# Kernel tuning notes

Measured on AMD Instinct MI355X. Metric: run time of the kernel, lower is better.

## Reference

```python
import jax, jax.numpy as jnp
import numpy as np

DIM = 128
B, H, W = 2, 256, 256


def conv2d(x, w, b, groups=1):
    # x: [B,C,H,W], w: [O, C//groups, kh, kw] (OIHW)
    y = jax.lax.conv_general_dilated(
        x, w, window_strides=(1, 1), padding='SAME',
        dimension_numbers=('NCHW', 'OIHW', 'NCHW'),
        feature_group_count=groups)
    return y + b[None, :, None, None]


def l2_normalize(x, axis=-1, eps=1e-12):
    # matches torch.nn.functional.normalize (p=2)
    n = jnp.sqrt(jnp.sum(x * x, axis=axis, keepdims=True))
    return x / jnp.maximum(n, eps)


def setup_inputs() -> dict:
    key = jax.random.key(0)
    ks = jax.random.split(key, 14)
    d = DIM
    h = d // 2
    s = 0.05
    return {
        'x': jax.random.normal(ks[0], (B, d, H, W), dtype=jnp.float32),
        'w_qkv': jax.random.normal(ks[1], (3 * d, d, 1, 1), dtype=jnp.float32) * s,
        'b_qkv': jax.random.normal(ks[2], (3 * d,), dtype=jnp.float32) * s,
        'w_q': jax.random.normal(ks[3], (d, 1, 3, 3), dtype=jnp.float32) * s,
        'b_q': jax.random.normal(ks[4], (d,), dtype=jnp.float32) * s,
        'w_k': jax.random.normal(ks[5], (d, 1, 3, 3), dtype=jnp.float32) * s,
        'b_k': jax.random.normal(ks[6], (d,), dtype=jnp.float32) * s,
        'w_v1': jax.random.normal(ks[7], (h, 2, 3, 3), dtype=jnp.float32) * s,  # groups=d/2, 2 in-ch per group
        'b_v1': jax.random.normal(ks[8], (h,), dtype=jnp.float32) * s,
        'w_v2': jax.random.normal(ks[9], (h, 1, 3, 3), dtype=jnp.float32) * s,  # depthwise on d/2
        'b_v2': jax.random.normal(ks[10], (h,), dtype=jnp.float32) * s,
        'temperature': jnp.ones((d, 1, 1), dtype=jnp.float32),
        'w_po': jax.random.normal(ks[11], (d, d, 1, 1), dtype=jnp.float32) * s,
        'b_po': jax.random.normal(ks[12], (d,), dtype=jnp.float32) * s,
    }


def reference(x, w_qkv, b_qkv, w_q, b_q, w_k, b_k, w_v1, b_v1, w_v2, b_v2,
              temperature, w_po, b_po):
    d = x.shape[1]
    h = d // 2
    # 1x1 conv -> qkv, then split
    qkv = conv2d(x, w_qkv, b_qkv)                     # [B,3d,H,W]
    q, k, v = jnp.split(qkv, 3, axis=1)
    # depthwise 3x3 on q, k
    q = conv2d(q, w_q, b_q, groups=d)
    k = conv2d(k, w_k, b_k, groups=d)
    # MDC on v: grouped conv (2->1 per group), depthwise, concat, sigmoid gate
    x1 = conv2d(v, w_v1, b_v1, groups=h)              # [B,d/2,H,W]
    x2 = conv2d(x1, w_v2, b_v2, groups=h)             # [B,d/2,H,W]
    v = jax.nn.sigmoid(v) * jnp.concatenate([x1, x2], axis=1)
    # per-channel row attention: normalize over W, [B,C,H,H] scores
    q1 = l2_normalize(q, axis=-1)
    k1 = l2_normalize(k, axis=-1)
    scores = jnp.einsum('bchw,bcgw->bchg', q1, k1) * temperature[None]  # [B,C,H,H]
    attn = jax.nn.softmax(scores, axis=-1)
    out = jnp.einsum('bchg,bcgw->bchw', attn, v)      # [B,C,H,W]
    return conv2d(out, w_po, b_po)
```

## Files before the change

### kernel.cpp

```cpp
#include <hip/hip_runtime.h>

typedef unsigned short u16;
typedef unsigned int u32;

#define HW 256
#define PIX 65536

#define WS_T1   100663296ull
#define WS_K1   134217728ull
#define WS_VP   167772160ull
#define WS_NEED 201326592ull

typedef __attribute__((ext_vector_type(8))) short s8v;
typedef __attribute__((ext_vector_type(4))) float f4v;

__device__ __forceinline__ float bu2f(u16 u){ union{u32 i; float f;} x; x.i=((u32)u)<<16; return x.f; }
__device__ __forceinline__ u16 f2bu(float f){ union{float f; u32 i;} x; x.f=f; u32 i=x.i; return (u16)((i + 0x7FFFu + ((i>>16)&1u))>>16); }
__device__ __forceinline__ float sigm(float x){ return 1.0f/(1.0f+__expf(-x)); }
__device__ __forceinline__ u16 cvt_el(float v){ return f2bu(v); }
__device__ __forceinline__ u16 cvt_el(u16 v){ return v; }
__device__ __forceinline__ int swz(int r, int c){ return r*256 + (((c>>3) ^ (r&7))<<3) + (c&7); }
__device__ __forceinline__ int pswz(int p, int c){ return (p<<7) + (((c>>3) ^ (p&7))<<3) + (c&7); }
__device__ __forceinline__ int vt_el(int w, int gb){
  int q = (w & 15) ^ gb ^ ((w >> 4) & 7);
  return ((w >> 4) << 10) + (gb << 7) + (q << 3);
}

__global__ __launch_bounds__(256) void k_wprep(const float* __restrict__ Wg, u16* __restrict__ G, int n){
  int i = blockIdx.x * 256 + threadIdx.x;
  if (i >= n) return;
  int o = i >> 7, c = i & 127;
  G[(o << 7) | (c ^ ((o & 7) << 3))] = f2bu(Wg[i]);
}

template<int OC, typename TIN, bool F32>
__global__ __launch_bounds__(512,1) void k_gemmP2(const TIN* __restrict__ in, const u16* __restrict__ Wbf,
                                                  const float* __restrict__ bias, int O_total,
                                                  void* __restrict__ outv){
  extern __shared__ u16 lds[];
  u16* Wl = lds;
  u16* Xl = lds + OC*128;
  int t = threadIdx.x;
  {
    const uint4* Wq4 = (const uint4*)Wbf;
    uint4* Wl4 = (uint4*)Wl;
    #pragma unroll
    for (int i = t; i < OC*16; i += 512) Wl4[i] = Wq4[i];
  }
  int p_blk = blockIdx.x * 256;
  int b = p_blk >> 16;
  int p0 = p_blk & 65535;
  if (sizeof(TIN) == 4){
    int p = t & 255, half = (t >> 8) * 64;
    const float* col = (const float*)in + ((size_t)(b*128 + half))*PIX + p0 + p;
    #pragma unroll
    for (int c8 = 0; c8 < 8; ++c8){
      u32 pk[4];
      #pragma unroll
      for (int j = 0; j < 4; ++j){
        u16 v0 = f2bu(col[(size_t)(c8*8 + 2*j)*PIX]);
        u16 v1 = f2bu(col[(size_t)(c8*8 + 2*j + 1)*PIX]);
        pk[j] = (u32)v0 | ((u32)v1 << 16);
      }
      *(uint4*)(Xl + pswz(p, half + c8*8)) = make_uint4(pk[0],pk[1],pk[2],pk[3]);
    }
  } else {
    int p = (t & 127) * 2, quarter = (t >> 7) * 32;
    const u16* col = (const u16*)in + ((size_t)(b*128 + quarter))*PIX + p0 + p;
    #pragma unroll
    for (int c8 = 0; c8 < 4; ++c8){
      u32 va[4], vb[4];
      #pragma unroll
      for (int j = 0; j < 4; ++j){
        u32 w0 = *(const u32*)(col + (size_t)(c8*8 + 2*j)*PIX);
        u32 w1 = *(const u32*)(col + (size_t)(c8*8 + 2*j + 1)*PIX);
        va[j] = (w0 & 0xFFFFu) | (w1 << 16);
        vb[j] = (w0 >> 16) | (w1 & 0xFFFF0000u);
      }
      *(uint4*)(Xl + pswz(p,     quarter + c8*8)) = make_uint4(va[0],va[1],va[2],va[3]);
      *(uint4*)(Xl + pswz(p + 1, quarter + c8*8)) = make_uint4(vb[0],vb[1],vb[2],vb[3]);
    }
  }
  __syncthreads();

  int wv = t >> 6, l = t & 63;
  int lg = l >> 4, lr = l & 15;
  int p_in0 = p0 + wv*32 + lr;

  s8v bf[2][4];
  #pragma unroll
  for (int pt = 0; pt < 2; ++pt){
    int p = wv*32 + pt*16 + lr;
    #pragma unroll
    for (int ks = 0; ks < 4; ++ks)
      bf[pt][ks] = *(const s8v*)(Xl + pswz(p, ks*32 + lg*8));
  }

  for (int ot = 0; ot < OC / 16; ++ot){
    f4v acc[2];
    acc[0] = (f4v){0.f,0.f,0.f,0.f};
    acc[1] = (f4v){0.f,0.f,0.f,0.f};
    int o = (ot << 4) + lr;
    const u16* wl = Wl + (o << 7);
    int sw = (o & 7) << 3;
    #pragma unroll
    for (int ks = 0; ks < 4; ++ks){
      s8v a = *(const s8v*)(wl + ((((ks << 5) + (lg << 3)) ^ sw)));
      acc[0] = __builtin_amdgcn_mfma_f32_16x16x32_bf16(a, bf[0][ks], acc[0], 0, 0, 0);
      acc[1] = __builtin_amdgcn_mfma_f32_16x16x32_bf16(a, bf[1][ks], acc[1], 0, 0, 0);
    }
    #pragma unroll
    for (int j = 0; j < 4; ++j){
      int o_row = (ot << 4) + (lg << 2) + j;
      float bv = bias[o_row];
      size_t base = ((size_t)(b * O_total + o_row)) << 16;
      #pragma unroll
      for (int pt = 0; pt < 2; ++pt){
        if (F32){
          ((float*)outv)[base + p_in0 + pt*16] = acc[pt][j] + bv;
        } else {
          ((u16*)outv)[base + p_in0 + pt*16] = f2bu(acc[pt][j] + bv);
        }
      }
    }
  }
}
#define GP384_LDS ((384*128 + 256*128) * 2)
#define GP128_LDS ((128*128 + 256*128) * 2)

__global__ __launch_bounds__(256) void k_dwqk2(const u16* __restrict__ qkv,
                                               const float* __restrict__ w_q, const float* __restrict__ b_q,
                                               const float* __restrict__ w_k, const float* __restrict__ b_k,
                                               u16* __restrict__ q1, u16* __restrict__ k1){
  __shared__ u16 ins[18*272];
  int t = threadIdx.x;
  int chunk = blockIdx.x;
  int c = blockIdx.y;
  int which = blockIdx.z & 1, b = blockIdx.z >> 1;
  const u16* in = qkv + ((size_t)(b*384 + which*128 + c)) * PIX;

  #pragma unroll
  for (int i = t; i < 612; i += 256) ((uint4*)ins)[i] = make_uint4(0,0,0,0);
  __syncthreads();
  int r0 = chunk*16 - 1;
  for (int i = t; i < 576; i += 256){
    int j = i >> 5, k = i & 31;
    int r = r0 + j;
    if (r >= 0 && r < HW)
      *(uint4*)(ins + j*272 + 8 + k*8) = *(const uint4*)(in + r*HW + k*8);
  }
  __syncthreads();

  const float* wk = (which ? w_k : w_q) + c*9;
  float K0=wk[0],K1=wk[1],K2=wk[2],K3=wk[3],K4=wk[4],K5=wk[5],K6=wk[6],K7=wk[7],K8=wk[8];
  float bias = (which ? b_k : b_q)[c];

  int wv = t >> 6, l = t & 63;
  int cb = l * 4;
  float wr[3][6];
  auto ldrow = [&](int j, int slot){
    ushort4 m = *(const ushort4*)(ins + j*272 + 8 + cb);
    wr[slot][0] = bu2f(ins[j*272 + 7 + cb]);
    wr[slot][1] = bu2f(m.x); wr[slot][2] = bu2f(m.y);
    wr[slot][3] = bu2f(m.z); wr[slot][4] = bu2f(m.w);
    wr[slot][5] = bu2f(ins[j*272 + 12 + cb]);
  };
  int rb = wv * 4;
  ldrow(rb, 0); ldrow(rb+1, 1);
  u16* outp = (which ? k1 : q1) + ((size_t)(b*128 + c)) * PIX;
  #pragma unroll
  for (int s = 0; s < 4; ++s){
    ldrow(rb + s + 2, (s+2)%3);
    const float* T = wr[s%3];
    const float* M = wr[(s+1)%3];
    const float* Bo = wr[(s+2)%3];
    float o[4]; float ss = 0.f;
    #pragma unroll
    for (int d = 0; d < 4; ++d){
      float a = bias;
      a = fmaf(K0, T[d], a);  a = fmaf(K1, T[d+1], a);  a = fmaf(K2, T[d+2], a);
      a = fmaf(K3, M[d], a);  a = fmaf(K4, M[d+1], a);  a = fmaf(K5, M[d+2], a);
      a = fmaf(K6, Bo[d], a); a = fmaf(K7, Bo[d+1], a); a = fmaf(K8, Bo[d+2], a);
      o[d] = a;
      ss = fmaf(a, a, ss);
    }
    #pragma unroll
    for (int m = 1; m < 64; m <<= 1) ss += __shfl_xor(ss, m, 64);
    float sc = 1.0f / fmaxf(sqrtf(ss), 1e-12f);
    int row = chunk*16 + rb + s;
    ushort4 pk;
    pk.x = f2bu(o[0]*sc); pk.y = f2bu(o[1]*sc); pk.z = f2bu(o[2]*sc); pk.w = f2bu(o[3]*sc);
    *(ushort4*)(outp + row*HW + cb) = pk;
  }
}

#define MDC_LDS (2*36*272*2 + 34*272*4)

__global__ __launch_bounds__(256,1) void k_mdc2(const u16* __restrict__ qkv,
                                                const float* __restrict__ w_v1, const float* __restrict__ b_v1,
                                                const float* __restrict__ w_v2, const float* __restrict__ b_v2,
                                                u16* __restrict__ vp){
  extern __shared__ char sm[];
  u16*   ins = (u16*)sm;
  float* x1s = (float*)(sm + 2*36*272*2);
  int t = threadIdx.x;
  int chunk = blockIdx.x;
  int g = blockIdx.y;
  int b = blockIdx.z;
  const u16* vbase = qkv + ((size_t)(b*384 + 256)) * PIX;

  #pragma unroll
  for (int i = t; i < 2*36*34; i += 256) ((uint4*)ins)[i] = make_uint4(0,0,0,0);
  for (int i = t; i < 34*68; i += 256) ((uint4*)x1s)[i] = make_uint4(0,0,0,0);
  __syncthreads();
  int r0 = chunk*32 - 2;
  #pragma unroll
  for (int ch = 0; ch < 2; ++ch){
    const u16* src = vbase + (size_t)(2*g + ch) * PIX;
    for (int i = t; i < 1152; i += 256){
      int j = i >> 5, k = i & 31;
      int r = r0 + j;
      if (r >= 0 && r < HW)
        *(uint4*)(ins + ch*36*272 + j*272 + 8 + k*8) = *(const uint4*)(src + r*HW + k*8);
    }
  }
  __syncthreads();

  float W1[18];
  #pragma unroll
  for (int i = 0; i < 18; ++i) W1[i] = w_v1[g*18 + i];
  float B1 = b_v1[g];
  int cb = t + 8;
  float win[2][3][3];
  #pragma unroll
  for (int ch = 0; ch < 2; ++ch)
    #pragma unroll
    for (int rr = 0; rr < 2; ++rr)
      #pragma unroll
      for (int k = 0; k < 3; ++k)
        win[ch][rr][k] = bu2f(ins[ch*36*272 + rr*272 + cb - 1 + k]);
  #pragma unroll
  for (int j = 0; j < 34; ++j){
    #pragma unroll
    for (int ch = 0; ch < 2; ++ch)
      #pragma unroll
      for (int k = 0; k < 3; ++k)
        win[ch][(j+2)%3][k] = bu2f(ins[ch*36*272 + (j+2)*272 + cb - 1 + k]);
    float v = B1;
    #pragma unroll
    for (int ch = 0; ch < 2; ++ch)
      #pragma unroll
      for (int i = 0; i < 3; ++i)
        #pragma unroll
        for (int k = 0; k < 3; ++k)
          v = fmaf(W1[ch*9 + i*3 + k], win[ch][(j+i)%3][k], v);
    int gr = chunk*32 - 1 + j;
    if (gr >= 0 && gr < HW) x1s[j*272 + cb] = v;
  }
  __syncthreads();

  float W2[9];
  #pragma unroll
  for (int i = 0; i < 9; ++i) W2[i] = w_v2[g*9 + i];
  float B2 = b_v2[g];
  const u16* vg   = vbase + (size_t)g * PIX;
  const u16* vg64 = vbase + (size_t)(64 + g) * PIX;
  u16* out0 = vp + ((size_t)(b*128 + g)) * PIX;
  u16* out1 = vp + ((size_t)(b*128 + 64 + g)) * PIX;
  float xw[3][3];
  #pragma unroll
  for (int rr = 0; rr < 2; ++rr)
    #pragma unroll
    for (int k = 0; k < 3; ++k)
      xw[rr][k] = x1s[rr*272 + cb - 1 + k];
  #pragma unroll
  for (int h = 0; h < 32; ++h){
    #pragma unroll
    for (int k = 0; k < 3; ++k)
      xw[(h+2)%3][k] = x1s[(h+2)*272 + cb - 1 + k];
    float x2 = B2;
    #pragma unroll
    for (int i = 0; i < 3; ++i)
      #pragma unroll
      for (int k = 0; k < 3; ++k)
        x2 = fmaf(W2[i*3 + k], xw[(h+i)%3][k], x2);
    int gr = chunk*32 + h;
    float g1 = sigm(bu2f(vg[gr*HW + t]));
    float g2 = sigm(bu2f(vg64[gr*HW + t]));
    float x1c = xw[(h+1)%3][1];
    out0[gr*HW + t] = f2bu(g1 * x1c);
    out1[gr*HW + t] = f2bu(g2 * x2);
  }
}

#define AT2_LDS 163840

__global__ __launch_bounds__(512,1) void k_attn2(const u16* __restrict__ q1, const u16* __restrict__ k1,
                                                 const u16* __restrict__ vp, const float* __restrict__ temp,
                                                 u16* __restrict__ out){
  extern __shared__ char smemraw[];
  u16* Qs = (u16*)smemraw;
  u16* Ks = Qs + 32768;
  u16* Ps = Ks + 16384;
  const int t = threadIdx.x;
  const int l = t & 63;
  const int wv = t >> 6;
  const int c15 = l & 15, h = l >> 4;
  const int blk = blockIdx.x;
  const int plane = blk >> 1, hf = blk & 1;
  const u16* qp  = q1 + (size_t)plane * PIX + hf*128*HW;
  const u16* kp  = k1 + (size_t)plane * PIX;
  const u16* vpp = vp + (size_t)plane * PIX;
  u16* op = out + (size_t)plane * PIX + hf*128*HW;
  const float tc = temp[plane & 127];

  #pragma unroll
  for (int i = 0; i < 8; ++i){
    int c = t + i*512; int row = c >> 5, bc = (c & 31) << 3;
    *(uint4*)(Qs + swz(row, bc)) = *(const uint4*)(qp + row*HW + bc);
  }
  #pragma unroll
  for (int i = 0; i < 4; ++i){
    int c = t + i*512; int row = c >> 5, bc = (c & 31) << 3;
    *(uint4*)(Ks + swz(row, bc)) = *(const uint4*)(kp + row*HW + bc);
  }
  __syncthreads();

  const int r_a = wv*16 + c15;
  s8v qa[8];
  #pragma unroll
  for (int ks = 0; ks < 8; ++ks)
    qa[ks] = *(const s8v*)(Qs + swz(r_a, ks*32 + h*8));

  f4v sacc[16];
  #pragma unroll
  for (int i = 0; i < 16; ++i) sacc[i] = (f4v){0.f,0.f,0.f,0.f};

  uint4 pf[4];
  #pragma unroll
  for (int gt = 0; gt < 4; ++gt){
    {
      const u16* src = (gt < 3) ? (kp + (gt+1)*64*HW) : vpp;
      #pragma unroll
      for (int i = 0; i < 4; ++i){
        int c = t + i*512; int row = c >> 5, bc = (c & 31) << 3;
        pf[i] = *(const uint4*)(src + row*HW + bc);
      }
    }
    #pragma unroll
    for (int gi = 0; gi < 4; ++gi){
      f4v acc = sacc[gt*4 + gi];
      #pragma unroll
      for (int ks = 0; ks < 8; ++ks){
        s8v b = *(const s8v*)(Ks + swz(gi*16 + c15, ks*32 + h*8));
        acc = __builtin_amdgcn_mfma_f32_16x16x32_bf16(qa[ks], b, acc, 0, 0, 0);
      }
      sacc[gt*4 + gi] = acc;
    }
    __syncthreads();
    #pragma unroll
    for (int i = 0; i < 4; ++i){
      int c = t + i*512; int row = c >> 5, bc = (c & 31) << 3;
      *(uint4*)(Ks + swz(row, bc)) = pf[i];
    }
    __syncthreads();
  }

  float mj[4] = {-1e30f,-1e30f,-1e30f,-1e30f};
  #pragma unroll
  for (int i = 0; i < 16; ++i)
    #pragma unroll
    for (int j = 0; j < 4; ++j){
      sacc[i][j] *= tc;
      mj[j] = fmaxf(mj[j], sacc[i][j]);
    }
  #pragma unroll
  for (int j = 0; j < 4; ++j){
    mj[j] = fmaxf(mj[j], __shfl_xor(mj[j], 1, 64));
    mj[j] = fmaxf(mj[j], __shfl_xor(mj[j], 2, 64));
    mj[j] = fmaxf(mj[j], __shfl_xor(mj[j], 4, 64));
    mj[j] = fmaxf(mj[j], __shfl_xor(mj[j], 8, 64));
  }
  float sj[4] = {0.f,0.f,0.f,0.f};
  #pragma unroll
  for (int i = 0; i < 16; ++i)
    #pragma unroll
    for (int j = 0; j < 4; ++j){
      float e = __expf(sacc[i][j] - mj[j]);
      sacc[i][j] = e;
      sj[j] += e;
    }
  #pragma unroll
  for (int j = 0; j < 4; ++j){
    sj[j] += __shfl_xor(sj[j], 1, 64);
    sj[j] += __shfl_xor(sj[j], 2, 64);
    sj[j] += __shfl_xor(sj[j], 4, 64);
    sj[j] += __shfl_xor(sj[j], 8, 64);
    sj[j] = 1.0f / sj[j];
  }
  #pragma unroll
  for (int i = 0; i < 16; ++i)
    #pragma unroll
    for (int j = 0; j < 4; ++j)
      Ps[swz(wv*16 + h*4 + j, i*16 + c15)] = f2bu(sacc[i][j] * sj[j]);
  __syncthreads();

  f4v oacc[16];
  #pragma unroll
  for (int i = 0; i < 16; ++i) oacc[i] = (f4v){0.f,0.f,0.f,0.f};

  #pragma unroll
  for (int gt = 0; gt < 4; ++gt){
    if (gt < 3){
      #pragma unroll
      for (int i = 0; i < 4; ++i){
        int c = t + i*512; int row = c >> 5, bc = (c & 31) << 3;
        pf[i] = *(const uint4*)(vpp + (gt+1)*64*HW + row*HW + bc);
      }
    }
    if (t < 256){
      int gb = t >> 5, wb = t & 31;
      u32 rr[8][4];
      #pragma unroll
      for (int i = 0; i < 8; ++i){
        uint4 v = *(const uint4*)(Ks + (gb*8 + i)*256 + ((wb ^ i) << 3));
        rr[i][0] = v.x; rr[i][1] = v.y; rr[i][2] = v.z; rr[i][3] = v.w;
      }
      #pragma unroll
      for (int j = 0; j < 8; ++j){
        u32 sel = (j & 1) ? 0x07060302u : 0x05040100u;
        int jh = j >> 1;
        u32 o0 = __builtin_amdgcn_perm(rr[1][jh], rr[0][jh], sel);
        u32 o1 = __builtin_amdgcn_perm(rr[3][jh], rr[2][jh], sel);
        u32 o2 = __builtin_amdgcn_perm(rr[5][jh], rr[4][jh], sel);
        u32 o3 = __builtin_amdgcn_perm(rr[7][jh], rr[6][jh], sel);
        int w = wb*8 + j;
        *(uint4*)(Qs + vt_el(w, gb)) = make_uint4(o0, o1, o2, o3);
      }
    }
    __syncthreads();
    if (gt < 3){
      #pragma unroll
      for (int i = 0; i < 4; ++i){
        int c = t + i*512; int row = c >> 5, bc = (c & 31) << 3;
        *(uint4*)(Ks + swz(row, bc)) = pf[i];
      }
    }
    s8v pa[2];
    #pragma unroll
    for (int k2 = 0; k2 < 2; ++k2)
      pa[k2] = *(const s8v*)(Ps + swz(r_a, gt*64 + k2*32 + h*8));
    #pragma unroll
    for (int wt = 0; wt < 16; ++wt){
      f4v acc = oacc[wt];
      #pragma unroll
      for (int k2 = 0; k2 < 2; ++k2){
        int w = wt*16 + c15;
        s8v b = *(const s8v*)(Qs + vt_el(w, (k2 << 2) + h));
        acc = __builtin_amdgcn_mfma_f32_16x16x32_bf16(pa[k2], b, acc, 0, 0, 0);
      }
      oacc[wt] = acc;
    }
    __syncthreads();
  }

  #pragma unroll
  for (int wt = 0; wt < 16; ++wt)
    #pragma unroll
    for (int j = 0; j < 4; ++j)
      Qs[swz(wv*16 + h*4 + j, wt*16 + c15)] = f2bu(oacc[wt][j]);
  __syncthreads();
  #pragma unroll
  for (int i = 0; i < 8; ++i){
    int row = wv*16 + i*2 + (l >> 5);
    int bc = (l & 31) << 3;
    uint4 v = *(const uint4*)(Qs + swz(row, bc));
    *(uint4*)(op + row*HW + bc) = v;
  }
}

extern "C" void kernel_launch(void* const* d_in, const int* in_sizes, int n_in,
                              void* d_out, int out_size, void* d_ws, size_t ws_size,
                              hipStream_t stream){
  (void)in_sizes; (void)n_in; (void)out_size;
  if (ws_size < (size_t)WS_NEED) return;

  const float* x     = (const float*)d_in[0];
  const float* w_qkv = (const float*)d_in[1];
  const float* b_qkv = (const float*)d_in[2];
  const float* w_q   = (const float*)d_in[3];
  const float* b_q   = (const float*)d_in[4];
  const float* w_k   = (const float*)d_in[5];
  const float* b_k   = (const float*)d_in[6];
  const float* w_v1  = (const float*)d_in[7];
  const float* b_v1  = (const float*)d_in[8];
  const float* w_v2  = (const float*)d_in[9];
  const float* b_v2  = (const float*)d_in[10];
  const float* temp  = (const float*)d_in[11];
  const float* w_po  = (const float*)d_in[12];
  const float* b_po  = (const float*)d_in[13];

  char* ws = (char*)d_ws;
  u16*  qkv = (u16*)ws;
  u16*  q1  = (u16*)(ws + WS_T1);
  u16*  k1  = (u16*)(ws + WS_K1);
  u16*  vp  = (u16*)(ws + WS_VP);
  u16*  aout = qkv;
  u16*  wq_bf  = q1;
  u16*  wpo_bf = k1;
  float* out = (float*)d_out;

  (void)hipFuncSetAttribute((const void*)k_gemmP2<384, float, false>, hipFuncAttributeMaxDynamicSharedMemorySize, GP384_LDS);
  (void)hipFuncSetAttribute((const void*)k_gemmP2<128, u16, true>,   hipFuncAttributeMaxDynamicSharedMemorySize, GP128_LDS);

  k_wprep<<<192, 256, 0, stream>>>(w_qkv, wq_bf, 384*128);
  k_gemmP2<384, float, false><<<512, 512, GP384_LDS, stream>>>(x, wq_bf, b_qkv, 384, (void*)qkv);
  k_dwqk2<<<dim3(16, 128, 4), 256, 0, stream>>>(qkv, w_q, b_q, w_k, b_k, q1, k1);
  (void)hipFuncSetAttribute((const void*)k_mdc2, hipFuncAttributeMaxDynamicSharedMemorySize, MDC_LDS);
  k_mdc2<<<dim3(8, 64, 2), 256, MDC_LDS, stream>>>(qkv, w_v1, b_v1, w_v2, b_v2, vp);
  (void)hipFuncSetAttribute((const void*)k_attn2, hipFuncAttributeMaxDynamicSharedMemorySize, AT2_LDS);
  k_attn2<<<512, 512, AT2_LDS, stream>>>(q1, k1, vp, temp, aout);
  k_wprep<<<64, 256, 0, stream>>>(w_po, wpo_bf, 128*128);
  k_gemmP2<128, u16, true><<<512, 512, GP128_LDS, stream>>>(aout, wpo_bf, b_po, 128, (void*)out);
}
```

Measured before the change: 233.5 us.

## Pre-transpose V in separate kernel and split attention into quarter-plane blocks

Adds a kernel that transposes the gated V planes in global memory, so the attention kernel no longer does the in-LDS perm-based transpose before each PV tile. The attention kernel now uses 256-thread blocks that each handle 64 query rows (1024 blocks), loads Q straight into registers instead of staging it in LDS, and cuts LDS to 64KB. Each block still reloads the full K and V per plane, so global traffic for K and V doubles. The extra transpose kernel adds one more launch and a read plus write of V.

```diff
diff --git a/kernel.cpp b/kernel.cpp
--- a/kernel.cpp
+++ b/kernel.cpp
@@ -21,16 +21,34 @@
 __device__ __forceinline__ u16 cvt_el(u16 v){ return v; }
 __device__ __forceinline__ int swz(int r, int c){ return r*256 + (((c>>3) ^ (r&7))<<3) + (c&7); }
 __device__ __forceinline__ int pswz(int p, int c){ return (p<<7) + (((c>>3) ^ (p&7))<<3) + (c&7); }
-__device__ __forceinline__ int vt_el(int w, int gb){
-  int q = (w & 15) ^ gb ^ ((w >> 4) & 7);
-  return ((w >> 4) << 10) + (gb << 7) + (q << 3);
-}
+__device__ __forceinline__ int vswz(int w, int gb){ return (w<<6) + ((gb ^ (w&7))<<3); }
 
 __global__ __launch_bounds__(256) void k_wprep(const float* __restrict__ Wg, u16* __restrict__ G, int n){
   int i = blockIdx.x * 256 + threadIdx.x;
   if (i >= n) return;
   int o = i >> 7, c = i & 127;
   G[(o << 7) | (c ^ ((o & 7) << 3))] = f2bu(Wg[i]);
+}
+
+__global__ __launch_bounds__(256) void k_trv(const u16* __restrict__ vp, u16* __restrict__ vpT){
+  __shared__ u16 tl[64*66];
+  int t = threadIdx.x;
+  int tile = blockIdx.x, plane = blockIdx.y;
+  int h0 = (tile >> 2) << 6, w0 = (tile & 3) << 6;
+  const u16* ip = vp + (size_t)plane * PIX;
+  int r = t >> 2, c0 = (t & 3) << 4;
+  u16 v[16];
+  *(uint4*)(v)   = *(const uint4*)(ip + (h0 + r)*HW + w0 + c0);
+  *(uint4*)(v+8) = *(const uint4*)(ip + (h0 + r)*HW + w0 + c0 + 8);
+  #pragma unroll
+  for (int j = 0; j < 16; ++j) tl[(c0 + j)*66 + r] = v[j];
+  __syncthreads();
+  u16 o[16];
+  #pragma unroll
+  for (int j = 0; j < 16; ++j) o[j] = tl[r*66 + c0 + j];
+  u16* opr = vpT + (size_t)plane * PIX + (w0 + r)*HW + h0 + c0;
+  *(uint4*)(opr)     = *(uint4*)(o);
+  *(uint4*)(opr + 8) = *(uint4*)(o + 8);
 }
 
 template<int OC, typename TIN, bool F32>
@@ -293,58 +311,57 @@
   }
 }
 
-#define AT2_LDS 163840
-
-__global__ __launch_bounds__(512,1) void k_attn2(const u16* __restrict__ q1, const u16* __restrict__ k1,
-                                                 const u16* __restrict__ vp, const float* __restrict__ temp,
+#define AT5_LDS 65536
+
+__global__ __launch_bounds__(256,1) void k_attn5(const u16* __restrict__ q1, const u16* __restrict__ k1,
+                                                 const u16* __restrict__ vpT, const float* __restrict__ temp,
                                                  u16* __restrict__ out){
-  extern __shared__ char smemraw[];
-  u16* Qs = (u16*)smemraw;
-  u16* Ks = Qs + 32768;
-  u16* Ps = Ks + 16384;
+  extern __shared__ char sm5[];
+  u16* KV = (u16*)sm5;
+  u16* Ps = (u16*)(sm5 + 32768);
   const int t = threadIdx.x;
   const int l = t & 63;
   const int wv = t >> 6;
   const int c15 = l & 15, h = l >> 4;
-  const int blk = blockIdx.x;
-  const int plane = blk >> 1, hf = blk & 1;
-  const u16* qp  = q1 + (size_t)plane * PIX + hf*128*HW;
+  const int n = blockIdx.x;
+  const int plane = n >> 2, qtr = n & 3;
+  const u16* qp  = q1 + (size_t)plane * PIX + qtr*64*HW;
   const u16* kp  = k1 + (size_t)plane * PIX;
-  const u16* vpp = vp + (size_t)plane * PIX;
-  u16* op = out + (size_t)plane * PIX + hf*128*HW;
+  const u16* vtp = vpT + (size_t)plane * PIX;
+  u16* op = out + (size_t)plane * PIX + qtr*64*HW;
   const float tc = temp[plane & 127];
 
+  const int r_a = wv*16 + c15;
+  const u16* qrow = qp + r_a*HW;
+  s8v qa[8];
+  #pragma unroll
+  for (int ks = 0; ks < 8; ++ks) qa[ks] = *(const s8v*)(qrow + ks*32 + h*8);
+
   #pragma unroll
   for (int i = 0; i < 8; ++i){
-    int c = t + i*512; int row = c >> 5, bc = (c & 31) << 3;
-    *(uint4*)(Qs + swz(row, bc)) = *(const uint4*)(qp + row*HW + bc);
-  }
-  #pragma unroll
-  for (int i = 0; i < 4; ++i){
-    int c = t + i*512; int row = c >> 5, bc = (c & 31) << 3;
-    *(uint4*)(Ks + swz(row, bc)) = *(const uint4*)(kp + row*HW + bc);
-  }
-  __syncthreads();
-
-  const int r_a = wv*16 + c15;
-  s8v qa[8];
-  #pragma unroll
-  for (int ks = 0; ks < 8; ++ks)
-    qa[ks] = *(const s8v*)(Qs + swz(r_a, ks*32 + h*8));
+    int idx = t + i*256; int row = idx >> 5, bc = (idx & 31) << 3;
+    *(uint4*)(KV + swz(row, bc)) = *(const uint4*)(kp + row*HW + bc);
+  }
+  __syncthreads();
 
   f4v sacc[16];
   #pragma unroll
   for (int i = 0; i < 16; ++i) sacc[i] = (f4v){0.f,0.f,0.f,0.f};
 
-  uint4 pf[4];
+  uint4 pf[8];
   #pragma unroll
   for (int gt = 0; gt < 4; ++gt){
-    {
-      const u16* src = (gt < 3) ? (kp + (gt+1)*64*HW) : vpp;
-      #pragma unroll
-      for (int i = 0; i < 4; ++i){
-        int c = t + i*512; int row = c >> 5, bc = (c & 31) << 3;
-        pf[i] = *(const uint4*)(src + row*HW + bc);
+    if (gt < 3){
+      #pragma unroll
+      for (int i = 0; i < 8; ++i){
+        int idx = t + i*256; int row = idx >> 5, bc = (idx & 31) << 3;
+        pf[i] = *(const uint4*)(kp + (gt+1)*64*HW + row*HW + bc);
+      }
+    } else {
+      #pragma unroll
+      for (int i = 0; i < 8; ++i){
+        int idx = t + i*256; int w = idx >> 3, gb = idx & 7;
+        pf[i] = *(const uint4*)(vtp + w*HW + gb*8);
       }
     }
     #pragma unroll
@@ -352,16 +369,24 @@
       f4v acc = sacc[gt*4 + gi];
       #pragma unroll
       for (int ks = 0; ks < 8; ++ks){
-        s8v b = *(const s8v*)(Ks + swz(gi*16 + c15, ks*32 + h*8));
+        s8v b = *(const s8v*)(KV + swz(gi*16 + c15, ks*32 + h*8));
         acc = __builtin_amdgcn_mfma_f32_16x16x32_bf16(qa[ks], b, acc, 0, 0, 0);
       }
       sacc[gt*4 + gi] = acc;
     }
     __syncthreads();
-    #pragma unroll
-    for (int i = 0; i < 4; ++i){
-      int c = t + i*512; int row = c >> 5, bc = (c & 31) << 3;
-      *(uint4*)(Ks + swz(row, bc)) = pf[i];
+    if (gt < 3){
+      #pragma unroll
+      for (int i = 0; i < 8; ++i){
+        int idx = t + i*256; int row = idx >> 5, bc = (idx & 31) << 3;
+        *(uint4*)(KV + swz(row, bc)) = pf[i];
+      }
+    } else {
+      #pragma unroll
+      for (int i = 0; i < 8; ++i){
+        int idx = t + i*256; int w = idx >> 3, gb = idx & 7;
+        *(uint4*)(KV + vswz(w, gb)) = pf[i];
+      }
     }
     __syncthreads();
   }
@@ -403,7 +428,6 @@
     #pragma unroll
     for (int j = 0; j < 4; ++j)
       Ps[swz(wv*16 + h*4 + j, i*16 + c15)] = f2bu(sacc[i][j] * sj[j]);
-  __syncthreads();
 
   f4v oacc[16];
   #pragma unroll
@@ -413,37 +437,9 @@
   for (int gt = 0; gt < 4; ++gt){
     if (gt < 3){
       #pragma unroll
-      for (int i = 0; i < 4; ++i){
-        int c = t + i*512; int row = c >> 5, bc = (c & 31) << 3;
-        pf[i] = *(const uint4*)(vpp + (gt+1)*64*HW + row*HW + bc);
-      }
-    }
-    if (t < 256){
-      int gb = t >> 5, wb = t & 31;
-      u32 rr[8][4];
-      #pragma unroll
       for (int i = 0; i < 8; ++i){
-        uint4 v = *(const uint4*)(Ks + (gb*8 + i)*256 + ((wb ^ i) << 3));
-        rr[i][0] = v.x; rr[i][1] = v.y; rr[i][2] = v.z; rr[i][3] = v.w;
-      }
-      #pragma unroll
-      for (int j = 0; j < 8; ++j){
-        u32 sel = (j & 1) ? 0x07060302u : 0x05040100u;
-        int jh = j >> 1;
-        u32 o0 = __builtin_amdgcn_perm(rr[1][jh], rr[0][jh], sel);
-        u32 o1 = __builtin_amdgcn_perm(rr[3][jh], rr[2][jh], sel);
-        u32 o2 = __builtin_amdgcn_perm(rr[5][jh], rr[4][jh], sel);
-        u32 o3 = __builtin_amdgcn_perm(rr[7][jh], rr[6][jh], sel);
-        int w = wb*8 + j;
-        *(uint4*)(Qs + vt_el(w, gb)) = make_uint4(o0, o1, o2, o3);
-      }
-    }
-    __syncthreads();
-    if (gt < 3){
-      #pragma unroll
-      for (int i = 0; i < 4; ++i){
-        int c = t + i*512; int row = c >> 5, bc = (c & 31) << 3;
-        *(uint4*)(Ks + swz(row, bc)) = pf[i];
+        int idx = t + i*256; int w = idx >> 3, gb = idx & 7;
+        pf[i] = *(const uint4*)(vtp + w*HW + (gt+1)*64 + gb*8);
       }
     }
     s8v pa[2];
@@ -455,27 +451,33 @@
       f4v acc = oacc[wt];
       #pragma unroll
       for (int k2 = 0; k2 < 2; ++k2){
-        int w = wt*16 + c15;
-        s8v b = *(const s8v*)(Qs + vt_el(w, (k2 << 2) + h));
+        s8v b = *(const s8v*)(KV + vswz(wt*16 + c15, (k2 << 2) + h));
         acc = __builtin_amdgcn_mfma_f32_16x16x32_bf16(pa[k2], b, acc, 0, 0, 0);
       }
       oacc[wt] = acc;
     }
-    __syncthreads();
-  }
-
+    if (gt < 3){
+      __syncthreads();
+      #pragma unroll
+      for (int i = 0; i < 8; ++i){
+        int idx = t + i*256; int w = idx >> 3, gb = idx & 7;
+        *(uint4*)(KV + vswz(w, gb)) = pf[i];
+      }
+      __syncthreads();
+    }
+  }
+
+  __syncthreads();
   #pragma unroll
   for (int wt = 0; wt < 16; ++wt)
     #pragma unroll
     for (int j = 0; j < 4; ++j)
-      Qs[swz(wv*16 + h*4 + j, wt*16 + c15)] = f2bu(oacc[wt][j]);
+      Ps[swz(wv*16 + h*4 + j, wt*16 + c15)] = f2bu(oacc[wt][j]);
   __syncthreads();
   #pragma unroll
   for (int i = 0; i < 8; ++i){
-    int row = wv*16 + i*2 + (l >> 5);
-    int bc = (l & 31) << 3;
-    uint4 v = *(const uint4*)(Qs + swz(row, bc));
-    *(uint4*)(op + row*HW + bc) = v;
+    int idx = t + i*256; int row = idx >> 5, bc = (idx & 31) << 3;
+    *(uint4*)(op + row*HW + bc) = *(const uint4*)(Ps + swz(row, bc));
   }
 }
 
@@ -506,20 +508,22 @@
   u16*  k1  = (u16*)(ws + WS_K1);
   u16*  vp  = (u16*)(ws + WS_VP);
   u16*  aout = qkv;
+  u16*  vpT = qkv + (size_t)256 * PIX;
   u16*  wq_bf  = q1;
   u16*  wpo_bf = k1;
   float* out = (float*)d_out;
 
   (void)hipFuncSetAttribute((const void*)k_gemmP2<384, float, false>, hipFuncAttributeMaxDynamicSharedMemorySize, GP384_LDS);
   (void)hipFuncSetAttribute((const void*)k_gemmP2<128, u16, true>,   hipFuncAttributeMaxDynamicSharedMemorySize, GP128_LDS);
+  (void)hipFuncSetAttribute((const void*)k_mdc2,  hipFuncAttributeMaxDynamicSharedMemorySize, MDC_LDS);
+  (void)hipFuncSetAttribute((const void*)k_attn5, hipFuncAttributeMaxDynamicSharedMemorySize, AT5_LDS);
 
   k_wprep<<<192, 256, 0, stream>>>(w_qkv, wq_bf, 384*128);
   k_gemmP2<384, float, false><<<512, 512, GP384_LDS, stream>>>(x, wq_bf, b_qkv, 384, (void*)qkv);
   k_dwqk2<<<dim3(16, 128, 4), 256, 0, stream>>>(qkv, w_q, b_q, w_k, b_k, q1, k1);
-  (void)hipFuncSetAttribute((const void*)k_mdc2, hipFuncAttributeMaxDynamicSharedMemorySize, MDC_LDS);
   k_mdc2<<<dim3(8, 64, 2), 256, MDC_LDS, stream>>>(qkv, w_v1, b_v1, w_v2, b_v2, vp);
-  (void)hipFuncSetAttribute((const void*)k_attn2, hipFuncAttributeMaxDynamicSharedMemorySize, AT2_LDS);
-  k_attn2<<<512, 512, AT2_LDS, stream>>>(q1, k1, vp, temp, aout);
+  k_trv<<<dim3(16, 256), 256, 0, stream>>>(vp, vpT);
+  k_attn5<<<1024, 256, AT5_LDS, stream>>>(q1, k1, vpT, temp, aout);
   k_wprep<<<64, 256, 0, stream>>>(w_po, wpo_bf, 128*128);
   k_gemmP2<128, u16, true><<<512, 512, GP128_LDS, stream>>>(aout, wpo_bf, b_po, 128, (void*)out);
 }
```

Result: slower. 288.9 us (+23.7%).
